# Kernel tuning notes

Hardware: AMD Instinct MI355X
Metric: run time of the kernel (lower is better)

Reference implementation:

```python
import jax, jax.numpy as jnp
import numpy as np

TEMPERATURE = 1.0
STRIDE = 1
PADDING = 2
RF = 5  # receptive_field_size
TREE_DEPTH = 3

# Each of the 16 binary difflogic ops op_g(a,b) is multilinear:
# op_g = c0 + c1*a + c2*b + c3*a*b. Rows ordered per the standard difflogic table:
# 0:0, 1:a&b, 2:a&~b, 3:a, 4:~a&b, 5:b, 6:xor, 7:or, 8:nor, 9:xnor,
# 10:~b, 11:a|~b, 12:~a, 13:~a|b, 14:nand, 15:1
_C = jnp.asarray(np.array([
    [0, 0, 0, 0],
    [0, 0, 0, 1],
    [0, 1, 0, -1],
    [0, 1, 0, 0],
    [0, 0, 1, -1],
    [0, 0, 1, 0],
    [0, 1, 1, -2],
    [0, 1, 1, -1],
    [1, -1, -1, 1],
    [1, -1, -1, 2],
    [1, 0, -1, 0],
    [1, 0, -1, 1],
    [1, -1, 0, 0],
    [1, -1, 0, 1],
    [1, 0, 0, -1],
    [1, 0, 0, 0]], dtype=np.float32))


def _gate(a, b, logits):
    """Soft LUT gate. a,b: (B,K,N,P); logits: (N,K,16) -> (B,K,N,P)."""
    w = jax.nn.softmax(logits / TEMPERATURE, axis=-1)          # (N,K,16)
    coef = jnp.einsum('nkg,gc->knc', w, _C)                    # (K,N,4)
    c = coef[None, :, :, None, :]                              # (1,K,N,1,4)
    return c[..., 0] + c[..., 1] * a + c[..., 2] * b + c[..., 3] * (a * b)


def setup_inputs() -> dict:
    key = jax.random.key(0)
    ks = jax.random.split(key, 8)
    B, Cin, H, W = 16, 32, 64, 64
    K, N = 64, 2 ** TREE_DEPTH  # num_kernels, leaf gates per tree
    x = jax.random.uniform(ks[0], (B, Cin, H, W), dtype=jnp.float32)
    idx_h = jax.random.randint(ks[1], (2, K, N), 0, RF, dtype=jnp.int32)
    idx_w = jax.random.randint(ks[2], (2, K, N), 0, RF, dtype=jnp.int32)
    idx_c = jax.random.randint(ks[3], (2, K, N), 0, Cin, dtype=jnp.int32)
    w0 = jax.random.normal(ks[4], (8, K, 16), dtype=jnp.float32)
    w1 = jax.random.normal(ks[5], (4, K, 16), dtype=jnp.float32)
    w2 = jax.random.normal(ks[6], (2, K, 16), dtype=jnp.float32)
    w3 = jax.random.normal(ks[7], (1, K, 16), dtype=jnp.float32)
    return {"x": x, "idx_h": idx_h, "idx_w": idx_w, "idx_c": idx_c,
            "w0": w0, "w1": w1, "w2": w2, "w3": w3}


def reference(x, idx_h, idx_w, idx_c, w0, w1, w2, w3):
    B, Cin, H, W = x.shape
    xp = jnp.pad(x, ((0, 0), (0, 0), (PADDING, PADDING), (PADDING, PADDING)))
    out_h = (H + 2 * PADDING - RF) // STRIDE + 1
    out_w = (W + 2 * PADDING - RF) // STRIDE + 1
    # Absolute gather coords per (rank-slot, kernel, leaf-gate, out_y, out_x)
    abs_h = idx_h[..., None, None] + (jnp.arange(out_h) * STRIDE)[:, None]   # (2,K,N,oh,1)
    abs_w = idx_w[..., None, None] + (jnp.arange(out_w) * STRIDE)[None, :]   # (2,K,N,1,ow)
    cc = idx_c[..., None, None]                                              # (2,K,N,1,1)
    g = xp[:, cc, abs_h, abs_w]                                # (B,2,K,N,oh,ow)
    K, N = g.shape[2], g.shape[3]
    g = g.reshape(B, 2, K, N, out_h * out_w)                   # (B,2,K,N,P)
    cur = _gate(g[:, 0], g[:, 1], w0)                          # (B,K,8,P) leaf level
    for wl in (w1, w2, w3):                                    # reduce tree: 8->4->2->1
        cur = _gate(cur[:, :, 0::2, :], cur[:, :, 1::2, :], wl)
    return cur.reshape(B, K, out_h, out_w)
```

## Files before the change

kernel.cpp:

```cpp
#include <hip/hip_runtime.h>
#include <hip/hip_bf16.h>

#define CIN 32
#define HW 64
#define KK 64
#define NLEAF 8
#define PADDING 2
#define TT 8
#define WS 12
#define WPOS (CIN * WS * WS)

typedef float f32x2 __attribute__((ext_vector_type(2)));

__device__ __constant__ float d_C[16][4] = {
    {0, 0, 0, 0},  {0, 0, 0, 1},  {0, 1, 0, -1}, {0, 1, 0, 0},
    {0, 0, 1, -1}, {0, 0, 1, 0},  {0, 1, 1, -2}, {0, 1, 1, -1},
    {1, -1, -1, 1},{1, -1, -1, 2},{1, 0, -1, 0}, {1, 0, -1, 1},
    {1, -1, 0, 0}, {1, -1, 0, 1}, {1, 0, 0, -1}, {1, 0, 0, 0}
};

__global__ __launch_bounds__(256) void prep_kernel(
    const int* __restrict__ idx_h, const int* __restrict__ idx_w, const int* __restrict__ idx_c,
    const float* __restrict__ w0, const float* __restrict__ w1,
    const float* __restrict__ w2, const float* __restrict__ w3,
    float* __restrict__ coefA, int* __restrict__ loffA)
{
    int tid = blockIdx.x * 256 + threadIdx.x;

    {
        int k = tid >> 4, j = tid & 15;
        int s = j & 1, leaf = j >> 1;
        int o = s * (KK * NLEAF) + k * NLEAF + leaf;
        loffA[tid] = idx_c[o] * (WS * WS) + idx_h[o] * WS + idx_w[o];
    }

    if (tid < KK * 15) {
        int k = tid / 15, node = tid % 15;
        const float* wp; int n;
        if (node < 8)       { wp = w0; n = node; }
        else if (node < 12) { wp = w1; n = node - 8; }
        else if (node < 14) { wp = w2; n = node - 12; }
        else                { wp = w3; n = 0; }
        const float4* lp = (const float4*)(wp + (size_t)(n * KK + k) * 16);
        float4 L0 = lp[0], L1 = lp[1], L2 = lp[2], L3 = lp[3];
        float l[16] = {L0.x, L0.y, L0.z, L0.w, L1.x, L1.y, L1.z, L1.w,
                       L2.x, L2.y, L2.z, L2.w, L3.x, L3.y, L3.z, L3.w};
        float m = l[0];
        #pragma unroll
        for (int g = 1; g < 16; ++g) m = fmaxf(m, l[g]);
        float p[16], s = 0.f;
        #pragma unroll
        for (int g = 0; g < 16; ++g) { p[g] = __expf(l[g] - m); s += p[g]; }
        float inv = 1.f / s;
        float c0 = 0, c1 = 0, c2 = 0, c3 = 0;
        #pragma unroll
        for (int g = 0; g < 16; ++g) {
            float w = p[g] * inv;
            c0 = fmaf(w, d_C[g][0], c0);
            c1 = fmaf(w, d_C[g][1], c1);
            c2 = fmaf(w, d_C[g][2], c2);
            c3 = fmaf(w, d_C[g][3], c3);
        }
        float* o = coefA + (k * 60 + node * 4);
        o[0] = c0; o[1] = c1; o[2] = c2; o[3] = c3;
    }
}

__device__ __forceinline__ f32x2 bc(float s) { return (f32x2){s, s}; }
__device__ __forceinline__ f32x2 gate2(const float* c, f32x2 a, f32x2 b) {
    return __builtin_elementwise_fma(b,
               __builtin_elementwise_fma(a, bc(c[3]), bc(c[2])),
               __builtin_elementwise_fma(a, bc(c[1]), bc(c[0])));
}

__global__ __launch_bounds__(512, 8) void logic_conv_kernel(
    const float* __restrict__ x, const int* __restrict__ loffA,
    const float* __restrict__ coefA, float* __restrict__ out)
{
    __shared__ f32x2 xt[WPOS];

    int tid = threadIdx.x;
    int bp  = blockIdx.x & 7;
    int rem = blockIdx.x >> 3;
    int t   = rem & 63;
    int kh  = rem >> 6;
    int r0  = (t >> 3) * TT;
    int c0  = (t & 7) * TT;

    const float* xb0 = x + (size_t)(2 * bp) * (CIN * HW * HW);
    const float* xb1 = xb0 + (CIN * HW * HW);

    #pragma unroll
    for (int i = 0; i < 9; ++i) {
        int e  = tid + i * 512;
        int c  = e / (WS * WS);
        int r  = e - c * (WS * WS);
        int rr = r / WS;
        int cc = r - rr * WS;
        int ih = r0 + rr - PADDING, iw = c0 + cc - PADDING;
        f32x2 v = {0.f, 0.f};
        if ((unsigned)ih < HW && (unsigned)iw < HW) {
            int go = (c * HW + ih) * HW + iw;
            v.x = xb0[go];
            v.y = xb1[go];
        }
        xt[e] = v;
    }
    __syncthreads();

    int lane = tid & 63, wave = tid >> 6;
    int tr = lane >> 3, tc = lane & 7;
    int pxe   = tr * WS + tc;
    int pxout = (r0 + tr) * HW + (c0 + tc);
    float* outB0 = out + ((size_t)(2 * bp) << 18);
    float* outB1 = outB0 + (1 << 18);

    int kbase = __builtin_amdgcn_readfirstlane(kh * 32 + wave * 4);

    #pragma unroll 2
    for (int i = 0; i < 4; ++i) {
        int k = kbase + i;
        const int*   L = loffA + (k << 4);
        const float* C = coefA + k * 60;

        f32x2 v[8];
        #pragma unroll
        for (int n = 0; n < 8; ++n) {
            f32x2 ga = xt[L[2 * n]     + pxe];
            f32x2 gb = xt[L[2 * n + 1] + pxe];
            v[n] = gate2(C + 4 * n, ga, gb);
        }
        f32x2 u[4];
        #pragma unroll
        for (int n = 0; n < 4; ++n)
            u[n] = gate2(C + 32 + 4 * n, v[2 * n], v[2 * n + 1]);
        f32x2 t0 = gate2(C + 48, u[0], u[1]);
        f32x2 t1 = gate2(C + 52, u[2], u[3]);
        f32x2 r  = gate2(C + 56, t0, t1);

        int ko = (k << 12) + pxout;
        __builtin_nontemporal_store(r.x, &outB0[ko]);
        __builtin_nontemporal_store(r.y, &outB1[ko]);
    }
}

extern "C" void kernel_launch(void* const* d_in, const int* in_sizes, int n_in,
                              void* d_out, int out_size, void* d_ws, size_t ws_size,
                              hipStream_t stream) {
    const float* x     = (const float*)d_in[0];
    const int*   idx_h = (const int*)d_in[1];
    const int*   idx_w = (const int*)d_in[2];
    const int*   idx_c = (const int*)d_in[3];
    const float* w0    = (const float*)d_in[4];
    const float* w1    = (const float*)d_in[5];
    const float* w2    = (const float*)d_in[6];
    const float* w3    = (const float*)d_in[7];
    float* out   = (float*)d_out;

    float* coefA = (float*)d_ws;
    int*   loffA = (int*)((char*)d_ws + 16384);

    hipLaunchKernelGGL(prep_kernel, dim3(4), dim3(256), 0, stream,
                       idx_h, idx_w, idx_c, w0, w1, w2, w3, coefA, loffA);
    hipLaunchKernelGGL(logic_conv_kernel, dim3(1024), dim3(512), 0, stream,
                       x, loffA, coefA, out);
}
```

Before: 25.40 us.

## Pack four batch images per LDS element and cover all kernels per block

Each shared-memory element now holds four batch images (float4) instead of two, and each block processes all 64 kernels rather than half of them. The grid shrinks from 1024 to 256 blocks and the LDS tile grows to about 73 KB of dynamic shared memory. The goal is to amortize each gather index and coefficient load over more batch elements and to stop reloading the same input tile in two blocks. In exchange the grid drops to 256 blocks, which may underfill a GPU of this size, and occupancy falls. The leaf offset table is also reordered so the a-inputs come before the b-inputs.

```diff
diff --git a/kernel.cpp b/kernel.cpp
--- a/kernel.cpp
+++ b/kernel.cpp
@@ -10,7 +10,7 @@
 #define WS 12
 #define WPOS (CIN * WS * WS)
 
-typedef float f32x2 __attribute__((ext_vector_type(2)));
+typedef float f32x4 __attribute__((ext_vector_type(4)));
 
 __device__ __constant__ float d_C[16][4] = {
     {0, 0, 0, 0},  {0, 0, 0, 1},  {0, 1, 0, -1}, {0, 1, 0, 0},
@@ -28,8 +28,8 @@
     int tid = blockIdx.x * 256 + threadIdx.x;
 
     {
-        int k = tid >> 4, j = tid & 15;
-        int s = j & 1, leaf = j >> 1;
+        int k = tid >> 4, n = tid & 15;
+        int s = n >> 3, leaf = n & 7;
         int o = s * (KK * NLEAF) + k * NLEAF + leaf;
         loffA[tid] = idx_c[o] * (WS * WS) + idx_h[o] * WS + idx_w[o];
     }
@@ -66,29 +66,29 @@
     }
 }
 
-__device__ __forceinline__ f32x2 bc(float s) { return (f32x2){s, s}; }
-__device__ __forceinline__ f32x2 gate2(const float* c, f32x2 a, f32x2 b) {
+__device__ __forceinline__ f32x4 bc4(float s) { return (f32x4){s, s, s, s}; }
+__device__ __forceinline__ f32x4 gate4(const float* c, f32x4 a, f32x4 b) {
     return __builtin_elementwise_fma(b,
-               __builtin_elementwise_fma(a, bc(c[3]), bc(c[2])),
-               __builtin_elementwise_fma(a, bc(c[1]), bc(c[0])));
+               __builtin_elementwise_fma(a, bc4(c[3]), bc4(c[2])),
+               __builtin_elementwise_fma(a, bc4(c[1]), bc4(c[0])));
 }
 
-__global__ __launch_bounds__(512, 8) void logic_conv_kernel(
+__global__ __launch_bounds__(512, 4) void logic_conv_kernel(
     const float* __restrict__ x, const int* __restrict__ loffA,
     const float* __restrict__ coefA, float* __restrict__ out)
 {
-    __shared__ f32x2 xt[WPOS];
+    extern __shared__ f32x4 xt[];
 
-    int tid = threadIdx.x;
-    int bp  = blockIdx.x & 7;
-    int rem = blockIdx.x >> 3;
-    int t   = rem & 63;
-    int kh  = rem >> 6;
-    int r0  = (t >> 3) * TT;
-    int c0  = (t & 7) * TT;
+    int tid  = threadIdx.x;
+    int quad = blockIdx.x & 3;
+    int t    = blockIdx.x >> 2;
+    int r0   = (t >> 3) * TT;
+    int c0   = (t & 7) * TT;
 
-    const float* xb0 = x + (size_t)(2 * bp) * (CIN * HW * HW);
+    const float* xb0 = x + (size_t)(4 * quad) * (CIN * HW * HW);
     const float* xb1 = xb0 + (CIN * HW * HW);
+    const float* xb2 = xb1 + (CIN * HW * HW);
+    const float* xb3 = xb2 + (CIN * HW * HW);
 
     #pragma unroll
     for (int i = 0; i < 9; ++i) {
@@ -98,11 +98,13 @@
         int rr = r / WS;
         int cc = r - rr * WS;
         int ih = r0 + rr - PADDING, iw = c0 + cc - PADDING;
-        f32x2 v = {0.f, 0.f};
+        f32x4 v = {0.f, 0.f, 0.f, 0.f};
         if ((unsigned)ih < HW && (unsigned)iw < HW) {
             int go = (c * HW + ih) * HW + iw;
             v.x = xb0[go];
             v.y = xb1[go];
+            v.z = xb2[go];
+            v.w = xb3[go];
         }
         xt[e] = v;
     }
@@ -112,35 +114,41 @@
     int tr = lane >> 3, tc = lane & 7;
     int pxe   = tr * WS + tc;
     int pxout = (r0 + tr) * HW + (c0 + tc);
-    float* outB0 = out + ((size_t)(2 * bp) << 18);
+    float* outB0 = out + ((size_t)(4 * quad) << 18);
     float* outB1 = outB0 + (1 << 18);
+    float* outB2 = outB1 + (1 << 18);
+    float* outB3 = outB2 + (1 << 18);
 
-    int kbase = __builtin_amdgcn_readfirstlane(kh * 32 + wave * 4);
+    int kbase = __builtin_amdgcn_readfirstlane(wave << 3);
 
     #pragma unroll 2
-    for (int i = 0; i < 4; ++i) {
-        int k = kbase + i;
+    for (int j = 0; j < 8; ++j) {
+        int k = kbase + j;
         const int*   L = loffA + (k << 4);
         const float* C = coefA + k * 60;
 
-        f32x2 v[8];
+        f32x4 g[16];
         #pragma unroll
-        for (int n = 0; n < 8; ++n) {
-            f32x2 ga = xt[L[2 * n]     + pxe];
-            f32x2 gb = xt[L[2 * n + 1] + pxe];
-            v[n] = gate2(C + 4 * n, ga, gb);
-        }
-        f32x2 u[4];
+        for (int n = 0; n < 16; ++n)
+            g[n] = xt[L[n] + pxe];
+
+        f32x4 v[8];
+        #pragma unroll
+        for (int n = 0; n < 8; ++n)
+            v[n] = gate4(C + 4 * n, g[n], g[8 + n]);
+        f32x4 u[4];
         #pragma unroll
         for (int n = 0; n < 4; ++n)
-            u[n] = gate2(C + 32 + 4 * n, v[2 * n], v[2 * n + 1]);
-        f32x2 t0 = gate2(C + 48, u[0], u[1]);
-        f32x2 t1 = gate2(C + 52, u[2], u[3]);
-        f32x2 r  = gate2(C + 56, t0, t1);
+            u[n] = gate4(C + 32 + 4 * n, v[2 * n], v[2 * n + 1]);
+        f32x4 t0 = gate4(C + 48, u[0], u[1]);
+        f32x4 t1 = gate4(C + 52, u[2], u[3]);
+        f32x4 r  = gate4(C + 56, t0, t1);
 
         int ko = (k << 12) + pxout;
         __builtin_nontemporal_store(r.x, &outB0[ko]);
         __builtin_nontemporal_store(r.y, &outB1[ko]);
+        __builtin_nontemporal_store(r.z, &outB2[ko]);
+        __builtin_nontemporal_store(r.w, &outB3[ko]);
     }
 }
 
@@ -162,6 +170,7 @@
 
     hipLaunchKernelGGL(prep_kernel, dim3(4), dim3(256), 0, stream,
                        idx_h, idx_w, idx_c, w0, w1, w2, w3, coefA, loffA);
-    hipLaunchKernelGGL(logic_conv_kernel, dim3(1024), dim3(512), 0, stream,
+    hipLaunchKernelGGL(logic_conv_kernel, dim3(256), dim3(512),
+                       WPOS * sizeof(f32x4), stream,
                        x, loffA, coefA, out);
 }
```

After: 32.02 us. 1.26x slower.
